# Kernel optimization log

Measured on AMD Instinct MI355X. Metric: run time of the kernel, lower is better.

Reference implementation:

```python
import jax, jax.numpy as jnp
import numpy as np

N_HEAD = 32
N_GROUPS = 8
HEAD_DIM = 64
HPG = N_HEAD // N_GROUPS  # heads per group
D_MODEL = N_HEAD * HEAD_DIM
KV_DIM = N_GROUPS * HEAD_DIM


def _rope_tables(T, head_dim, dtype=jnp.float32):
    # theta_i = 10000^{-2i/d}; freqs[t, i] = t * theta_i  -> [T, head_dim//2]
    theta = 1.0 / (10000.0 ** (jnp.arange(0, head_dim, 2, dtype=jnp.float32) / head_dim))
    freqs = jnp.arange(T, dtype=jnp.float32)[:, None] * theta[None, :]
    return jnp.cos(freqs).astype(dtype), jnp.sin(freqs).astype(dtype)


def _apply_rope(x, cos, sin):
    # x: [B, H, T, D]; complex rotation on consecutive pairs of the last dim
    B, H, T, D = x.shape
    xs = x.reshape(B, H, T, D // 2, 2)
    a, b = xs[..., 0], xs[..., 1]
    c = cos[None, None, :, :]
    s = sin[None, None, :, :]
    ra = a * c - b * s
    rb = a * s + b * c
    return jnp.stack([ra, rb], axis=-1).reshape(B, H, T, D)


def setup_inputs() -> dict:
    key = jax.random.key(0)
    k1, k2, k3 = jax.random.split(key, 3)
    B, T = 2, 2048
    x = jax.random.normal(k1, (B, T, D_MODEL), dtype=jnp.float32)
    # Linear weights stored [in, out] (transpose of torch layout); bias=False
    w_qkv = jax.random.normal(k2, (D_MODEL, D_MODEL + 2 * KV_DIM), dtype=jnp.float32) * (D_MODEL ** -0.5)
    w_proj = jax.random.normal(k3, (D_MODEL, D_MODEL), dtype=jnp.float32) * (D_MODEL ** -0.5)
    return {"x": x, "w_qkv": w_qkv, "w_proj": w_proj}


def reference(x, w_qkv, w_proj):
    B, T, C = x.shape
    qkv = x @ w_qkv  # [B, T, C + 2*KV_DIM]
    q = qkv[..., :C].reshape(B, T, N_HEAD, HEAD_DIM).transpose(0, 2, 1, 3)        # [B,H,T,D]
    k = qkv[..., C:C + KV_DIM].reshape(B, T, N_GROUPS, HEAD_DIM).transpose(0, 2, 1, 3)  # [B,G,T,D]
    v = qkv[..., C + KV_DIM:].reshape(B, T, N_GROUPS, HEAD_DIM).transpose(0, 2, 1, 3)   # [B,G,T,D]
    cos, sin = _rope_tables(T, HEAD_DIM)
    q = _apply_rope(q, cos, sin)
    k = _apply_rope(k, cos, sin)
    # GQA: group queries by KV group instead of repeat_interleave on K/V
    qg = q.reshape(B, N_GROUPS, HPG, T, HEAD_DIM)
    scale = HEAD_DIM ** -0.5
    scores = jnp.einsum('bghqd,bgkd->bghqk', qg, k) * scale  # [B,G,HPG,T,T]
    causal = jnp.tril(jnp.ones((T, T), dtype=bool))
    scores = jnp.where(causal[None, None, None, :, :], scores, -jnp.inf)
    attn = jax.nn.softmax(scores, axis=-1)
    y = jnp.einsum('bghqk,bgkd->bghqd', attn, v)             # [B,G,HPG,T,D]
    y = y.reshape(B, N_HEAD, T, HEAD_DIM).transpose(0, 2, 1, 3).reshape(B, T, C)
    return y @ w_proj
```

## Files before the change

### kernel.cpp

```cpp
#include <hip/hip_runtime.h>
#include <math.h>

typedef float f32x4 __attribute__((ext_vector_type(4)));
typedef _Float16 half_t;
typedef half_t f16x4 __attribute__((ext_vector_type(4)));
typedef half_t f16x8 __attribute__((ext_vector_type(8)));

#define T_    2048
#define DM_   2048
#define KV_   1024
#define L2T_  0.4152410118609203f

#define CVT8(H,A,B) { H[0]=(half_t)(A)[0]; H[1]=(half_t)(A)[1]; H[2]=(half_t)(A)[2]; H[3]=(half_t)(A)[3]; \
                      H[4]=(half_t)(B)[0]; H[5]=(half_t)(B)[1]; H[6]=(half_t)(B)[2]; H[7]=(half_t)(B)[3]; }

#define GLOAD16(GP, LP) __builtin_amdgcn_global_load_lds( \
    (const __attribute__((address_space(1))) unsigned int*)(GP), \
    (__attribute__((address_space(3))) unsigned int*)(LP), 16, 0, 0)

__global__ __launch_bounds__(256) void cvt_f32_f16(
    const float* __restrict__ s, half_t* __restrict__ d, int n8){
  const int i = blockIdx.x * 256 + threadIdx.x;
  if (i >= n8) return;
  const f32x4 u = *(const f32x4*)(s + (size_t)i * 8);
  const f32x4 v = *(const f32x4*)(s + (size_t)i * 8 + 4);
  f16x8 h; CVT8(h, u, v);
  *(f16x8*)(d + (size_t)i * 8) = h;
}

__global__ __launch_bounds__(256) void transpose_cvt(
    const float* __restrict__ src, half_t* __restrict__ dst, int K, int N){
  __shared__ float tile[64][65];
  const int k0 = blockIdx.y * 64, n0 = blockIdx.x * 64;
  const int tx = threadIdx.x & 15, ty = threadIdx.x >> 4;
#pragma unroll
  for (int i = 0; i < 4; ++i){
    const f32x4 v = *(const f32x4*)&src[(size_t)(k0 + ty + 16 * i) * N + n0 + tx * 4];
    tile[ty + 16 * i][tx * 4 + 0] = v[0];
    tile[ty + 16 * i][tx * 4 + 1] = v[1];
    tile[ty + 16 * i][tx * 4 + 2] = v[2];
    tile[ty + 16 * i][tx * 4 + 3] = v[3];
  }
  __syncthreads();
#pragma unroll
  for (int i = 0; i < 4; ++i){
    f16x4 h;
    h[0] = (half_t)tile[tx * 4 + 0][ty + 16 * i];
    h[1] = (half_t)tile[tx * 4 + 1][ty + 16 * i];
    h[2] = (half_t)tile[tx * 4 + 2][ty + 16 * i];
    h[3] = (half_t)tile[tx * 4 + 3][ty + 16 * i];
    *(f16x4*)&dst[(size_t)(n0 + ty + 16 * i) * K + k0 + tx * 4] = h;
  }
}

__global__ __launch_bounds__(256) void rope_table(float* __restrict__ tab){
  const int idx = blockIdx.x * 256 + threadIdx.x;
  const int t = idx >> 5, i = idx & 31;
  float sv, cv;
  sincosf((float)t * exp2f(-(float)i * L2T_), &sv, &cv);
  tab[idx * 2]     = cv;
  tab[idx * 2 + 1] = sv;
}

__global__ __launch_bounds__(256) void gemm_qkv(
    const half_t* __restrict__ A16, const half_t* __restrict__ BT16,
    const float* __restrict__ tab,
    half_t* __restrict__ Cq, half_t* __restrict__ Ckv, int N, int K){
  __shared__ half_t Ah[128 * 64];
  __shared__ half_t Bh[128 * 64];
  const int tid = threadIdx.x;

  const int nwg = (int)(gridDim.x * gridDim.y);
  int lin = (int)blockIdx.y * (int)gridDim.x + (int)blockIdx.x;
  lin = (lin & 7) * (nwg >> 3) + (lin >> 3);
  const int m0 = (lin / (int)gridDim.x) * 128;
  const int n0 = (lin % (int)gridDim.x) * 128;

  const int lane = tid & 63, wid = tid >> 6;
  const int wr = wid >> 1, wc = wid & 1;
  const int fr = lane & 15, fg = lane >> 4;

  f32x4 acc[4][4];
#pragma unroll
  for (int i = 0; i < 4; ++i)
#pragma unroll
    for (int j = 0; j < 4; ++j) acc[i][j] = (f32x4){0.f, 0.f, 0.f, 0.f};

  const half_t* gA[4]; const half_t* gB[4]; half_t* lA[4]; half_t* lB[4];
#pragma unroll
  for (int r = 0; r < 4; ++r){
    const int q = r * 256 + tid;
    const int row = q >> 3, c = q & 7, cg = c ^ (row & 7);
    gA[r] = A16  + (size_t)(m0 + row) * K + cg * 8;
    gB[r] = BT16 + (size_t)(n0 + row) * K + cg * 8;
    lA[r] = &Ah[q * 8];
    lB[r] = &Bh[q * 8];
  }

  for (int kb = 0; kb < K; kb += 64){
    __syncthreads();
#pragma unroll
    for (int r = 0; r < 4; ++r){
      GLOAD16(gA[r] + kb, lA[r]);
      GLOAD16(gB[r] + kb, lB[r]);
    }
    __syncthreads();

#pragma unroll
    for (int kk = 0; kk < 2; ++kk){
      f16x8 bf[4];
#pragma unroll
      for (int j = 0; j < 4; ++j){
        const int brow = wc * 64 + j * 16 + fr;
        bf[j] = *(const f16x8*)&Bh[brow * 64 + ((kk * 4 + fg) ^ (brow & 7)) * 8];
      }
#pragma unroll
      for (int i = 0; i < 4; ++i){
        const int arow = wr * 64 + i * 16 + fr;
        const f16x8 af = *(const f16x8*)&Ah[arow * 64 + ((kk * 4 + fg) ^ (arow & 7)) * 8];
        acc[i][0] = __builtin_amdgcn_mfma_f32_16x16x32_f16(af, bf[0], acc[i][0], 0, 0, 0);
        acc[i][1] = __builtin_amdgcn_mfma_f32_16x16x32_f16(af, bf[1], acc[i][1], 0, 0, 0);
        acc[i][2] = __builtin_amdgcn_mfma_f32_16x16x32_f16(af, bf[2], acc[i][2], 0, 0, 0);
        acc[i][3] = __builtin_amdgcn_mfma_f32_16x16x32_f16(af, bf[3], acc[i][3], 0, 0, 0);
      }
    }
  }

  const int region = (n0 < DM_) ? 0 : ((n0 < DM_ + 512) ? 1 : 2);
  half_t* Cb = (region == 0) ? Cq : Ckv;
  const int stride = (region == 0) ? DM_ : KV_;
  const int cbase = (region == 0 ? n0 : n0 - DM_) + wc * 64 + fr;

  if (region < 2){
    const float scale = (region == 0) ? 0.125f : 1.f;
    const bool ev = ((fr & 1) == 0);
#pragma unroll
    for (int i = 0; i < 4; ++i){
      const int row = m0 + wr * 64 + i * 16 + fg * 4;
#pragma unroll
      for (int j = 0; j < 4; ++j){
        const int freq = (fr >> 1) + 8 * j;
#pragma unroll
        for (int r = 0; r < 4; ++r){
          const float v = acc[i][j][r];
          const float p = __shfl_xor(v, 1);
          const float* cs = tab + (size_t)(((row + r) & (T_ - 1)) * 32 + freq) * 2;
          const float o = v * cs[0] + cs[1] * (ev ? -p : p);
          Cb[(size_t)(row + r) * stride + cbase + j * 16] = (half_t)(o * scale);
        }
      }
    }
  } else {
#pragma unroll
    for (int i = 0; i < 4; ++i){
      const int row = m0 + wr * 64 + i * 16 + fg * 4;
#pragma unroll
      for (int j = 0; j < 4; ++j)
#pragma unroll
        for (int r = 0; r < 4; ++r)
          Cb[(size_t)(row + r) * stride + cbase + j * 16] = (half_t)acc[i][j][r];
    }
  }
}

__global__ __launch_bounds__(256) void gemm_proj(
    const half_t* __restrict__ A16, const half_t* __restrict__ BT16,
    float* __restrict__ C, int N, int K){
  __shared__ half_t Ah[128 * 64];
  __shared__ half_t Bh[128 * 64];
  const int tid = threadIdx.x;

  const int nwg = (int)(gridDim.x * gridDim.y);
  int lin = (int)blockIdx.y * (int)gridDim.x + (int)blockIdx.x;
  lin = (lin & 7) * (nwg >> 3) + (lin >> 3);
  const int m0 = (lin / (int)gridDim.x) * 128;
  const int n0 = (lin % (int)gridDim.x) * 128;

  const int lane = tid & 63, wid = tid >> 6;
  const int wr = wid >> 1, wc = wid & 1;
  const int fr = lane & 15, fg = lane >> 4;

  f32x4 acc[4][4];
#pragma unroll
  for (int i = 0; i < 4; ++i)
#pragma unroll
    for (int j = 0; j < 4; ++j) acc[i][j] = (f32x4){0.f, 0.f, 0.f, 0.f};

  const half_t* gA[4]; const half_t* gB[4]; half_t* lA[4]; half_t* lB[4];
#pragma unroll
  for (int r = 0; r < 4; ++r){
    const int q = r * 256 + tid;
    const int row = q >> 3, c = q & 7, cg = c ^ (row & 7);
    gA[r] = A16  + (size_t)(m0 + row) * K + cg * 8;
    gB[r] = BT16 + (size_t)(n0 + row) * K + cg * 8;
    lA[r] = &Ah[q * 8];
    lB[r] = &Bh[q * 8];
  }

  for (int kb = 0; kb < K; kb += 64){
    __syncthreads();
#pragma unroll
    for (int r = 0; r < 4; ++r){
      GLOAD16(gA[r] + kb, lA[r]);
      GLOAD16(gB[r] + kb, lB[r]);
    }
    __syncthreads();

#pragma unroll
    for (int kk = 0; kk < 2; ++kk){
      f16x8 bf[4];
#pragma unroll
      for (int j = 0; j < 4; ++j){
        const int brow = wc * 64 + j * 16 + fr;
        bf[j] = *(const f16x8*)&Bh[brow * 64 + ((kk * 4 + fg) ^ (brow & 7)) * 8];
      }
#pragma unroll
      for (int i = 0; i < 4; ++i){
        const int arow = wr * 64 + i * 16 + fr;
        const f16x8 af = *(const f16x8*)&Ah[arow * 64 + ((kk * 4 + fg) ^ (arow & 7)) * 8];
        acc[i][0] = __builtin_amdgcn_mfma_f32_16x16x32_f16(af, bf[0], acc[i][0], 0, 0, 0);
        acc[i][1] = __builtin_amdgcn_mfma_f32_16x16x32_f16(af, bf[1], acc[i][1], 0, 0, 0);
        acc[i][2] = __builtin_amdgcn_mfma_f32_16x16x32_f16(af, bf[2], acc[i][2], 0, 0, 0);
        acc[i][3] = __builtin_amdgcn_mfma_f32_16x16x32_f16(af, bf[3], acc[i][3], 0, 0, 0);
      }
    }
  }

#pragma unroll
  for (int i = 0; i < 4; ++i){
    const int row = m0 + wr * 64 + i * 16 + fg * 4;
#pragma unroll
    for (int j = 0; j < 4; ++j){
      const int col = n0 + wc * 64 + fr + j * 16;
#pragma unroll
      for (int r = 0; r < 4; ++r)
        C[(size_t)(row + r) * N + col] = acc[i][j][r];
    }
  }
}

#define LDQ 72
#define LDV 72
#define LDP 20
#define NT_ 32

#define SUMRED(V,S) { V[0]+=__shfl_xor(V[0],S); V[1]+=__shfl_xor(V[1],S); \
                      V[2]+=__shfl_xor(V[2],S); V[3]+=__shfl_xor(V[3],S); }
#define EXPC(SV) { SV[0]=__expf(SV[0]-4.f); SV[1]=__expf(SV[1]-4.f); \
                   SV[2]=__expf(SV[2]-4.f); SV[3]=__expf(SV[3]-4.f); }
#define PSTORE(SV,CB) { Ph[pw + (CB)*320 + (pr+0)*LDP + fr] = (half_t)SV[0]; \
                        Ph[pw + (CB)*320 + (pr+1)*LDP + fr] = (half_t)SV[1]; \
                        Ph[pw + (CB)*320 + (pr+2)*LDP + fr] = (half_t)SV[2]; \
                        Ph[pw + (CB)*320 + (pr+3)*LDP + fr] = (half_t)SV[3]; }

__global__ __launch_bounds__(256) void attn_flash_mfma(
    half_t* __restrict__ qy, const half_t* __restrict__ kv){
  __shared__ half_t Kh[64 * LDQ];
  __shared__ half_t Vt[64 * LDV];
  __shared__ half_t Ph[4 * 4 * 16 * LDP];
  const int tid = threadIdx.x;
  const int lane = tid & 63, w = tid >> 6;
  const int fr = lane & 15, fg = lane >> 4;
  const int bx = (int)blockIdx.x;
  const int h = blockIdx.y, b = blockIdx.z;
  const int g = h >> 2;
  const half_t* kbase = kv + (size_t)b * T_ * KV_ + g * 64;
  const half_t* vbase = kbase + 512;

  const int srow = tid >> 2, sc0 = (tid & 3) * 16;
  const int vd = tid & 63, vk8 = (tid >> 6) * 8;
  const int arow = (w * 16 + fr) * LDQ;
  const int pw = w * (4 * 16 * LDP);
  const int pr = fg * 4;

#pragma unroll 1
  for (int half = 0; half < 2; ++half){
    const int qt = half ? bx : (NT_ - 1 - bx);
    half_t* qbase = qy + ((size_t)b * T_ + qt * 64) * DM_ + h * 64;

    __syncthreads();
    {
      const half_t* src = qbase + (size_t)srow * DM_ + sc0;
      *(f16x8*)&Kh[srow * LDQ + sc0]     = *(const f16x8*)(src);
      *(f16x8*)&Kh[srow * LDQ + sc0 + 8] = *(const f16x8*)(src + 8);
    }
    __syncthreads();
    const f16x8 aq0 = *(const f16x8*)&Kh[arow + fg * 8];
    const f16x8 aq1 = *(const f16x8*)&Kh[arow + 32 + fg * 8];
    __syncthreads();

    f32x4 l = {0.f, 0.f, 0.f, 0.f};
    f32x4 o0 = {0.f,0.f,0.f,0.f}, o1 = {0.f,0.f,0.f,0.f};
    f32x4 o2 = {0.f,0.f,0.f,0.f}, o3 = {0.f,0.f,0.f,0.f};

    for (int kt = 0; kt <= qt; ++kt){
      {
        const half_t* src = kbase + (size_t)(kt * 64 + srow) * KV_ + sc0;
        *(f16x8*)&Kh[srow * LDQ + sc0]     = *(const f16x8*)(src);
        *(f16x8*)&Kh[srow * LDQ + sc0 + 8] = *(const f16x8*)(src + 8);
      }
#pragma unroll
      for (int it = 0; it < 2; ++it){
        const int k0 = vk8 + it * 32;
        const half_t* src = vbase + (size_t)(kt * 64 + k0) * KV_ + vd;
        f16x8 hv;
        hv[0] = src[0];
        hv[1] = src[KV_];
        hv[2] = src[2 * KV_];
        hv[3] = src[3 * KV_];
        hv[4] = src[4 * KV_];
        hv[5] = src[5 * KV_];
        hv[6] = src[6 * KV_];
        hv[7] = src[7 * KV_];
        *(f16x8*)&Vt[vd * LDV + k0] = hv;
      }
      __syncthreads();

      f32x4 s0 = {0.f,0.f,0.f,0.f}, s1 = {0.f,0.f,0.f,0.f};
      f32x4 s2 = {0.f,0.f,0.f,0.f}, s3 = {0.f,0.f,0.f,0.f};
      {
        const f16x8 b0 = *(const f16x8*)&Kh[(fr     ) * LDQ + fg * 8];
        const f16x8 b1 = *(const f16x8*)&Kh[(fr     ) * LDQ + 32 + fg * 8];
        s0 = __builtin_amdgcn_mfma_f32_16x16x32_f16(aq0, b0, s0, 0, 0, 0);
        s0 = __builtin_amdgcn_mfma_f32_16x16x32_f16(aq1, b1, s0, 0, 0, 0);
      }
      {
        const f16x8 b0 = *(const f16x8*)&Kh[(16 + fr) * LDQ + fg * 8];
        const f16x8 b1 = *(const f16x8*)&Kh[(16 + fr) * LDQ + 32 + fg * 8];
        s1 = __builtin_amdgcn_mfma_f32_16x16x32_f16(aq0, b0, s1, 0, 0, 0);
        s1 = __builtin_amdgcn_mfma_f32_16x16x32_f16(aq1, b1, s1, 0, 0, 0);
      }
      {
        const f16x8 b0 = *(const f16x8*)&Kh[(32 + fr) * LDQ + fg * 8];
        const f16x8 b1 = *(const f16x8*)&Kh[(32 + fr) * LDQ + 32 + fg * 8];
        s2 = __builtin_amdgcn_mfma_f32_16x16x32_f16(aq0, b0, s2, 0, 0, 0);
        s2 = __builtin_amdgcn_mfma_f32_16x16x32_f16(aq1, b1, s2, 0, 0, 0);
      }
      {
        const f16x8 b0 = *(const f16x8*)&Kh[(48 + fr) * LDQ + fg * 8];
        const f16x8 b1 = *(const f16x8*)&Kh[(48 + fr) * LDQ + 32 + fg * 8];
        s3 = __builtin_amdgcn_mfma_f32_16x16x32_f16(aq0, b0, s3, 0, 0, 0);
        s3 = __builtin_amdgcn_mfma_f32_16x16x32_f16(aq1, b1, s3, 0, 0, 0);
      }

      if (kt == qt){
        const int qr = w * 16 + fg * 4;
        if (fr      > qr    ) s0[0] = -1e30f;
        if (fr      > qr + 1) s0[1] = -1e30f;
        if (fr      > qr + 2) s0[2] = -1e30f;
        if (fr      > qr + 3) s0[3] = -1e30f;
        if (fr + 16 > qr    ) s1[0] = -1e30f;
        if (fr + 16 > qr + 1) s1[1] = -1e30f;
        if (fr + 16 > qr + 2) s1[2] = -1e30f;
        if (fr + 16 > qr + 3) s1[3] = -1e30f;
        if (fr + 32 > qr    ) s2[0] = -1e30f;
        if (fr + 32 > qr + 1) s2[1] = -1e30f;
        if (fr + 32 > qr + 2) s2[2] = -1e30f;
        if (fr + 32 > qr + 3) s2[3] = -1e30f;
        if (fr + 48 > qr    ) s3[0] = -1e30f;
        if (fr + 48 > qr + 1) s3[1] = -1e30f;
        if (fr + 48 > qr + 2) s3[2] = -1e30f;
        if (fr + 48 > qr + 3) s3[3] = -1e30f;
      }

      EXPC(s0); EXPC(s1); EXPC(s2); EXPC(s3);
      l += s0 + s1 + s2 + s3;

      PSTORE(s0, 0); PSTORE(s1, 1); PSTORE(s2, 2); PSTORE(s3, 3);

      const f16x8 pa0 = *(const f16x8*)&Ph[pw + ((fg >> 1)    ) * 320 + fr * LDP + (fg & 1) * 8];
      const f16x8 pa1 = *(const f16x8*)&Ph[pw + (2 + (fg >> 1)) * 320 + fr * LDP + (fg & 1) * 8];
      {
        const f16x8 b0 = *(const f16x8*)&Vt[(fr     ) * LDV + fg * 8];
        const f16x8 b1 = *(const f16x8*)&Vt[(fr     ) * LDV + 32 + fg * 8];
        o0 = __builtin_amdgcn_mfma_f32_16x16x32_f16(pa0, b0, o0, 0, 0, 0);
        o0 = __builtin_amdgcn_mfma_f32_16x16x32_f16(pa1, b1, o0, 0, 0, 0);
      }
      {
        const f16x8 b0 = *(const f16x8*)&Vt[(16 + fr) * LDV + fg * 8];
        const f16x8 b1 = *(const f16x8*)&Vt[(16 + fr) * LDV + 32 + fg * 8];
        o1 = __builtin_amdgcn_mfma_f32_16x16x32_f16(pa0, b0, o1, 0, 0, 0);
        o1 = __builtin_amdgcn_mfma_f32_16x16x32_f16(pa1, b1, o1, 0, 0, 0);
      }
      {
        const f16x8 b0 = *(const f16x8*)&Vt[(32 + fr) * LDV + fg * 8];
        const f16x8 b1 = *(const f16x8*)&Vt[(32 + fr) * LDV + 32 + fg * 8];
        o2 = __builtin_amdgcn_mfma_f32_16x16x32_f16(pa0, b0, o2, 0, 0, 0);
        o2 = __builtin_amdgcn_mfma_f32_16x16x32_f16(pa1, b1, o2, 0, 0, 0);
      }
      {
        const f16x8 b0 = *(const f16x8*)&Vt[(48 + fr) * LDV + fg * 8];
        const f16x8 b1 = *(const f16x8*)&Vt[(48 + fr) * LDV + 32 + fg * 8];
        o3 = __builtin_amdgcn_mfma_f32_16x16x32_f16(pa0, b0, o3, 0, 0, 0);
        o3 = __builtin_amdgcn_mfma_f32_16x16x32_f16(pa1, b1, o3, 0, 0, 0);
      }

      __syncthreads();
    }

    SUMRED(l, 1); SUMRED(l, 2); SUMRED(l, 4); SUMRED(l, 8);
    f32x4 inv;
    inv[0] = 1.f / l[0]; inv[1] = 1.f / l[1];
    inv[2] = 1.f / l[2]; inv[3] = 1.f / l[3];
    o0 *= inv; o1 *= inv; o2 *= inv; o3 *= inv;
    const int orow = w * 16 + fg * 4;
    half_t* dst = qbase + (size_t)orow * DM_ + fr;
    dst[(size_t)0 * DM_ +  0] = (half_t)o0[0]; dst[(size_t)1 * DM_ +  0] = (half_t)o0[1];
    dst[(size_t)2 * DM_ +  0] = (half_t)o0[2]; dst[(size_t)3 * DM_ +  0] = (half_t)o0[3];
    dst[(size_t)0 * DM_ + 16] = (half_t)o1[0]; dst[(size_t)1 * DM_ + 16] = (half_t)o1[1];
    dst[(size_t)2 * DM_ + 16] = (half_t)o1[2]; dst[(size_t)3 * DM_ + 16] = (half_t)o1[3];
    dst[(size_t)0 * DM_ + 32] = (half_t)o2[0]; dst[(size_t)1 * DM_ + 32] = (half_t)o2[1];
    dst[(size_t)2 * DM_ + 32] = (half_t)o2[2]; dst[(size_t)3 * DM_ + 32] = (half_t)o2[3];
    dst[(size_t)0 * DM_ + 48] = (half_t)o3[0]; dst[(size_t)1 * DM_ + 48] = (half_t)o3[1];
    dst[(size_t)2 * DM_ + 48] = (half_t)o3[2]; dst[(size_t)3 * DM_ + 48] = (half_t)o3[3];
  }
}

extern "C" void kernel_launch(void* const* d_in, const int* in_sizes, int n_in,
                              void* d_out, int out_size, void* d_ws, size_t ws_size,
                              hipStream_t stream) {
  const float *x = nullptr, *w_qkv = nullptr, *w_proj = nullptr;
  for (int i = 0; i < n_in; ++i){
    if (in_sizes[i] == 8388608)      x      = (const float*)d_in[i];
    else if (in_sizes[i] == 6291456) w_qkv  = (const float*)d_in[i];
    else if (in_sizes[i] == 4194304) w_proj = (const float*)d_in[i];
  }
  float* out = (float*)d_out;

  char* ws = (char*)d_ws;
  half_t* qy_h    = (half_t*)ws;
  half_t* kv_h    = (half_t*)(ws + (size_t)16777216);
  half_t* wqkvT   = (half_t*)(ws + (size_t)25165824);
  half_t* wprojT  = (half_t*)(ws + (size_t)37748736);
  float*  tab     = (float*) (ws + (size_t)46137344);
  half_t* x_h     = (half_t*)d_out;

  rope_table<<<256, 256, 0, stream>>>(tab);
  cvt_f32_f16<<<4096, 256, 0, stream>>>(x, x_h, 1048576);
  transpose_cvt<<<dim3(48, 32), 256, 0, stream>>>(w_qkv, wqkvT, 2048, 3072);
  transpose_cvt<<<dim3(32, 32), 256, 0, stream>>>(w_proj, wprojT, 2048, 2048);
  gemm_qkv<<<dim3(24, 32), 256, 0, stream>>>(x_h, wqkvT, tab, qy_h, kv_h, 3072, 2048);
  attn_flash_mfma<<<dim3(16, 32, 2), 256, 0, stream>>>(qy_h, kv_h);
  gemm_proj<<<dim3(16, 32), 256, 0, stream>>>(qy_h, wprojT, out, 2048, 2048);
}
```

Measured before the change: 327.2 us.

## Double-buffer GEMM LDS tiles and pre-transpose V for attention loads

Both GEMMs now use a double-buffered K=32 tile pipeline: the async global-to-LDS loads for the next tile are issued before computing the current one, which removes one barrier per iteration. The XOR swizzle is adapted to the new layout. A separate kernel transposes V once into a [B,G,D,T] buffer placed in the spare output memory. The attention kernel can then fill its Vt tile with vectorized 16-byte loads instead of strided scalar gathers. The trade-offs are an extra kernel launch and extra memory traffic for the transpose, and the smaller K tile means more loop iterations.

```diff
diff --git a/kernel.cpp b/kernel.cpp
--- a/kernel.cpp
+++ b/kernel.cpp
@@ -53,6 +53,30 @@
   }
 }
 
+__global__ __launch_bounds__(256) void v_transpose(
+    const half_t* __restrict__ kv, half_t* __restrict__ vT){
+  __shared__ half_t tile[64][72];
+  const int tt = blockIdx.x, g = blockIdx.y, b = blockIdx.z;
+  const int r = threadIdx.x >> 3;
+  const int c = (threadIdx.x & 7) * 8;
+  const half_t* src = kv + ((size_t)b * T_ + tt * 64) * KV_ + 512 + g * 64;
+#pragma unroll
+  for (int i = 0; i < 2; ++i){
+    const int row = r + 32 * i;
+    *(f16x8*)&tile[row][c] = *(const f16x8*)(src + (size_t)row * KV_ + c);
+  }
+  __syncthreads();
+  half_t* dst = vT + ((size_t)(b * 8 + g) * 64) * T_ + tt * 64;
+#pragma unroll
+  for (int i = 0; i < 2; ++i){
+    const int drow = r + 32 * i;
+    f16x8 h;
+#pragma unroll
+    for (int j = 0; j < 8; ++j) h[j] = tile[c + j][drow];
+    *(f16x8*)(dst + (size_t)drow * T_ + c) = h;
+  }
+}
+
 __global__ __launch_bounds__(256) void rope_table(float* __restrict__ tab){
   const int idx = blockIdx.x * 256 + threadIdx.x;
   const int t = idx >> 5, i = idx & 31;
@@ -62,12 +86,47 @@
   tab[idx * 2 + 1] = sv;
 }
 
+#define STAGE_G(dA, dB, KB) { \
+  GLOAD16(gA0 + (KB), (dA) + loff0); \
+  GLOAD16(gA1 + (KB), (dA) + loff1); \
+  GLOAD16(gB0 + (KB), (dB) + loff0); \
+  GLOAD16(gB1 + (KB), (dB) + loff1); }
+
+#define GEMM_PREAMBLE \
+  const int lane = tid & 63, wid = tid >> 6; \
+  const int wr = wid >> 1, wc = wid & 1; \
+  const int fr = lane & 15, fg = lane >> 4; \
+  const int srow16 = lane >> 2, schk = lane & 3; \
+  const int lrow0 = wid * 16 + srow16; \
+  const int lrow1 = (4 + wid) * 16 + srow16; \
+  const int loff0 = lrow0 * 32 + schk * 8; \
+  const int loff1 = lrow1 * 32 + schk * 8; \
+  const int gchk0 = schk ^ ((lrow0 >> 1) & 3); \
+  const int gchk1 = schk ^ ((lrow1 >> 1) & 3);
+
+#define GEMM_COMPUTE(CA, CB) { \
+  f16x8 bf[4]; \
+  _Pragma("unroll") \
+  for (int j = 0; j < 4; ++j){ \
+    const int brow = wc * 64 + j * 16 + fr; \
+    bf[j] = *(const f16x8*)&(CB)[brow * 32 + (fg ^ ((brow >> 1) & 3)) * 8]; \
+  } \
+  _Pragma("unroll") \
+  for (int i = 0; i < 4; ++i){ \
+    const int arow = wr * 64 + i * 16 + fr; \
+    const f16x8 af = *(const f16x8*)&(CA)[arow * 32 + (fg ^ ((arow >> 1) & 3)) * 8]; \
+    acc[i][0] = __builtin_amdgcn_mfma_f32_16x16x32_f16(af, bf[0], acc[i][0], 0, 0, 0); \
+    acc[i][1] = __builtin_amdgcn_mfma_f32_16x16x32_f16(af, bf[1], acc[i][1], 0, 0, 0); \
+    acc[i][2] = __builtin_amdgcn_mfma_f32_16x16x32_f16(af, bf[2], acc[i][2], 0, 0, 0); \
+    acc[i][3] = __builtin_amdgcn_mfma_f32_16x16x32_f16(af, bf[3], acc[i][3], 0, 0, 0); \
+  } }
+
 __global__ __launch_bounds__(256) void gemm_qkv(
     const half_t* __restrict__ A16, const half_t* __restrict__ BT16,
     const float* __restrict__ tab,
     half_t* __restrict__ Cq, half_t* __restrict__ Ckv, int N, int K){
-  __shared__ half_t Ah[128 * 64];
-  __shared__ half_t Bh[128 * 64];
+  __shared__ half_t Ah[2 * 128 * 32];
+  __shared__ half_t Bh[2 * 128 * 32];
   const int tid = threadIdx.x;
 
   const int nwg = (int)(gridDim.x * gridDim.y);
@@ -76,9 +135,7 @@
   const int m0 = (lin / (int)gridDim.x) * 128;
   const int n0 = (lin % (int)gridDim.x) * 128;
 
-  const int lane = tid & 63, wid = tid >> 6;
-  const int wr = wid >> 1, wc = wid & 1;
-  const int fr = lane & 15, fg = lane >> 4;
+  GEMM_PREAMBLE
 
   f32x4 acc[4][4];
 #pragma unroll
@@ -86,44 +143,21 @@
 #pragma unroll
     for (int j = 0; j < 4; ++j) acc[i][j] = (f32x4){0.f, 0.f, 0.f, 0.f};
 
-  const half_t* gA[4]; const half_t* gB[4]; half_t* lA[4]; half_t* lB[4];
-#pragma unroll
-  for (int r = 0; r < 4; ++r){
-    const int q = r * 256 + tid;
-    const int row = q >> 3, c = q & 7, cg = c ^ (row & 7);
-    gA[r] = A16  + (size_t)(m0 + row) * K + cg * 8;
-    gB[r] = BT16 + (size_t)(n0 + row) * K + cg * 8;
-    lA[r] = &Ah[q * 8];
-    lB[r] = &Bh[q * 8];
-  }
-
-  for (int kb = 0; kb < K; kb += 64){
+  const half_t* gA0 = A16  + (size_t)(m0 + lrow0) * K + gchk0 * 8;
+  const half_t* gA1 = A16  + (size_t)(m0 + lrow1) * K + gchk1 * 8;
+  const half_t* gB0 = BT16 + (size_t)(n0 + lrow0) * K + gchk0 * 8;
+  const half_t* gB1 = BT16 + (size_t)(n0 + lrow1) * K + gchk1 * 8;
+
+  half_t *cA = Ah, *nA = Ah + 4096, *cB = Bh, *nB = Bh + 4096;
+  STAGE_G(cA, cB, 0);
+  __syncthreads();
+  for (int kb = 0; kb < K; kb += 32){
+    if (kb + 32 < K) STAGE_G(nA, nB, kb + 32);
+    GEMM_COMPUTE(cA, cB);
     __syncthreads();
-#pragma unroll
-    for (int r = 0; r < 4; ++r){
-      GLOAD16(gA[r] + kb, lA[r]);
-      GLOAD16(gB[r] + kb, lB[r]);
-    }
-    __syncthreads();
-
-#pragma unroll
-    for (int kk = 0; kk < 2; ++kk){
-      f16x8 bf[4];
-#pragma unroll
-      for (int j = 0; j < 4; ++j){
-        const int brow = wc * 64 + j * 16 + fr;
-        bf[j] = *(const f16x8*)&Bh[brow * 64 + ((kk * 4 + fg) ^ (brow & 7)) * 8];
-      }
-#pragma unroll
-      for (int i = 0; i < 4; ++i){
-        const int arow = wr * 64 + i * 16 + fr;
-        const f16x8 af = *(const f16x8*)&Ah[arow * 64 + ((kk * 4 + fg) ^ (arow & 7)) * 8];
-        acc[i][0] = __builtin_amdgcn_mfma_f32_16x16x32_f16(af, bf[0], acc[i][0], 0, 0, 0);
-        acc[i][1] = __builtin_amdgcn_mfma_f32_16x16x32_f16(af, bf[1], acc[i][1], 0, 0, 0);
-        acc[i][2] = __builtin_amdgcn_mfma_f32_16x16x32_f16(af, bf[2], acc[i][2], 0, 0, 0);
-        acc[i][3] = __builtin_amdgcn_mfma_f32_16x16x32_f16(af, bf[3], acc[i][3], 0, 0, 0);
-      }
-    }
+    half_t* t;
+    t = cA; cA = nA; nA = t;
+    t = cB; cB = nB; nB = t;
   }
 
   const int region = (n0 < DM_) ? 0 : ((n0 < DM_ + 512) ? 1 : 2);
@@ -166,8 +200,8 @@
 __global__ __launch_bounds__(256) void gemm_proj(
     const half_t* __restrict__ A16, const half_t* __restrict__ BT16,
     float* __restrict__ C, int N, int K){
-  __shared__ half_t Ah[128 * 64];
-  __shared__ half_t Bh[128 * 64];
+  __shared__ half_t Ah[2 * 128 * 32];
+  __shared__ half_t Bh[2 * 128 * 32];
   const int tid = threadIdx.x;
 
   const int nwg = (int)(gridDim.x * gridDim.y);
@@ -176,9 +210,7 @@
   const int m0 = (lin / (int)gridDim.x) * 128;
   const int n0 = (lin % (int)gridDim.x) * 128;
 
-  const int lane = tid & 63, wid = tid >> 6;
-  const int wr = wid >> 1, wc = wid & 1;
-  const int fr = lane & 15, fg = lane >> 4;
+  GEMM_PREAMBLE
 
   f32x4 acc[4][4];
 #pragma unroll
@@ -186,44 +218,21 @@
 #pragma unroll
     for (int j = 0; j < 4; ++j) acc[i][j] = (f32x4){0.f, 0.f, 0.f, 0.f};
 
-  const half_t* gA[4]; const half_t* gB[4]; half_t* lA[4]; half_t* lB[4];
-#pragma unroll
-  for (int r = 0; r < 4; ++r){
-    const int q = r * 256 + tid;
-    const int row = q >> 3, c = q & 7, cg = c ^ (row & 7);
-    gA[r] = A16  + (size_t)(m0 + row) * K + cg * 8;
-    gB[r] = BT16 + (size_t)(n0 + row) * K + cg * 8;
-    lA[r] = &Ah[q * 8];
-    lB[r] = &Bh[q * 8];
-  }
-
-  for (int kb = 0; kb < K; kb += 64){
+  const half_t* gA0 = A16  + (size_t)(m0 + lrow0) * K + gchk0 * 8;
+  const half_t* gA1 = A16  + (size_t)(m0 + lrow1) * K + gchk1 * 8;
+  const half_t* gB0 = BT16 + (size_t)(n0 + lrow0) * K + gchk0 * 8;
+  const half_t* gB1 = BT16 + (size_t)(n0 + lrow1) * K + gchk1 * 8;
+
+  half_t *cA = Ah, *nA = Ah + 4096, *cB = Bh, *nB = Bh + 4096;
+  STAGE_G(cA, cB, 0);
+  __syncthreads();
+  for (int kb = 0; kb < K; kb += 32){
+    if (kb + 32 < K) STAGE_G(nA, nB, kb + 32);
+    GEMM_COMPUTE(cA, cB);
     __syncthreads();
-#pragma unroll
-    for (int r = 0; r < 4; ++r){
-      GLOAD16(gA[r] + kb, lA[r]);
-      GLOAD16(gB[r] + kb, lB[r]);
-    }
-    __syncthreads();
-
-#pragma unroll
-    for (int kk = 0; kk < 2; ++kk){
-      f16x8 bf[4];
-#pragma unroll
-      for (int j = 0; j < 4; ++j){
-        const int brow = wc * 64 + j * 16 + fr;
-        bf[j] = *(const f16x8*)&Bh[brow * 64 + ((kk * 4 + fg) ^ (brow & 7)) * 8];
-      }
-#pragma unroll
-      for (int i = 0; i < 4; ++i){
-        const int arow = wr * 64 + i * 16 + fr;
-        const f16x8 af = *(const f16x8*)&Ah[arow * 64 + ((kk * 4 + fg) ^ (arow & 7)) * 8];
-        acc[i][0] = __builtin_amdgcn_mfma_f32_16x16x32_f16(af, bf[0], acc[i][0], 0, 0, 0);
-        acc[i][1] = __builtin_amdgcn_mfma_f32_16x16x32_f16(af, bf[1], acc[i][1], 0, 0, 0);
-        acc[i][2] = __builtin_amdgcn_mfma_f32_16x16x32_f16(af, bf[2], acc[i][2], 0, 0, 0);
-        acc[i][3] = __builtin_amdgcn_mfma_f32_16x16x32_f16(af, bf[3], acc[i][3], 0, 0, 0);
-      }
-    }
+    half_t* t;
+    t = cA; cA = nA; nA = t;
+    t = cB; cB = nB; nB = t;
   }
 
 #pragma unroll
@@ -254,7 +263,8 @@
                         Ph[pw + (CB)*320 + (pr+3)*LDP + fr] = (half_t)SV[3]; }
 
 __global__ __launch_bounds__(256) void attn_flash_mfma(
-    half_t* __restrict__ qy, const half_t* __restrict__ kv){
+    half_t* __restrict__ qy, const half_t* __restrict__ kv,
+    const half_t* __restrict__ vT){
   __shared__ half_t Kh[64 * LDQ];
   __shared__ half_t Vt[64 * LDV];
   __shared__ half_t Ph[4 * 4 * 16 * LDP];
@@ -265,10 +275,10 @@
   const int h = blockIdx.y, b = blockIdx.z;
   const int g = h >> 2;
   const half_t* kbase = kv + (size_t)b * T_ * KV_ + g * 64;
-  const half_t* vbase = kbase + 512;
+  const half_t* vTb = vT + (size_t)(b * 8 + g) * 64 * T_;
 
   const int srow = tid >> 2, sc0 = (tid & 3) * 16;
-  const int vd = tid & 63, vk8 = (tid >> 6) * 8;
+  const int vrow = tid >> 2, vcol = (tid & 3) * 16;
   const int arow = (w * 16 + fr) * LDQ;
   const int pw = w * (4 * 16 * LDP);
   const int pr = fg * 4;
@@ -299,20 +309,10 @@
         *(f16x8*)&Kh[srow * LDQ + sc0]     = *(const f16x8*)(src);
         *(f16x8*)&Kh[srow * LDQ + sc0 + 8] = *(const f16x8*)(src + 8);
       }
-#pragma unroll
-      for (int it = 0; it < 2; ++it){
-        const int k0 = vk8 + it * 32;
-        const half_t* src = vbase + (size_t)(kt * 64 + k0) * KV_ + vd;
-        f16x8 hv;
-        hv[0] = src[0];
-        hv[1] = src[KV_];
-        hv[2] = src[2 * KV_];
-        hv[3] = src[3 * KV_];
-        hv[4] = src[4 * KV_];
-        hv[5] = src[5 * KV_];
-        hv[6] = src[6 * KV_];
-        hv[7] = src[7 * KV_];
-        *(f16x8*)&Vt[vd * LDV + k0] = hv;
+      {
+        const half_t* src = vTb + (size_t)vrow * T_ + kt * 64 + vcol;
+        *(f16x8*)&Vt[vrow * LDV + vcol]     = *(const f16x8*)(src);
+        *(f16x8*)&Vt[vrow * LDV + vcol + 8] = *(const f16x8*)(src + 8);
       }
       __syncthreads();
 
@@ -434,12 +434,14 @@
   half_t* wprojT  = (half_t*)(ws + (size_t)37748736);
   float*  tab     = (float*) (ws + (size_t)46137344);
   half_t* x_h     = (half_t*)d_out;
+  half_t* vT      = (half_t*)((char*)d_out + (size_t)16777216);
 
   rope_table<<<256, 256, 0, stream>>>(tab);
   cvt_f32_f16<<<4096, 256, 0, stream>>>(x, x_h, 1048576);
   transpose_cvt<<<dim3(48, 32), 256, 0, stream>>>(w_qkv, wqkvT, 2048, 3072);
   transpose_cvt<<<dim3(32, 32), 256, 0, stream>>>(w_proj, wprojT, 2048, 2048);
   gemm_qkv<<<dim3(24, 32), 256, 0, stream>>>(x_h, wqkvT, tab, qy_h, kv_h, 3072, 2048);
-  attn_flash_mfma<<<dim3(16, 32, 2), 256, 0, stream>>>(qy_h, kv_h);
+  v_transpose<<<dim3(32, 8, 2), 256, 0, stream>>>(kv_h, vT);
+  attn_flash_mfma<<<dim3(16, 32, 2), 256, 0, stream>>>(qy_h, kv_h, vT);
   gemm_proj<<<dim3(16, 32), 256, 0, stream>>>(qy_h, wprojT, out, 2048, 2048);
 }
```

Measured after the change: 325.7 us. About the same (-0.5%).
